# Optimization experiments

Measured on AMD Instinct MI355X. Metric: run time of the kernel, lower is better.

## Reference

```python
import jax, jax.numpy as jnp
import numpy as np

N_NODES = 50000
N_EDGES = 1600000
D = 128


def setup_inputs() -> dict:
    key = jax.random.key(0)
    ks = jax.random.split(key, 12)
    feats = jax.random.normal(ks[0], (N_NODES, D), dtype=jnp.float32)
    src = jax.random.randint(ks[1], (N_EDGES,), 0, N_NODES)
    dst = jax.random.randint(ks[2], (N_EDGES,), 0, N_NODES)
    s = 1.0 / np.sqrt(D)
    inp = {"feats": feats, "src": src, "dst": dst}
    for i, k0 in enumerate(range(3, 12, 3)):
        inp[f"w_self{i}"] = jax.random.normal(ks[k0], (D, D), dtype=jnp.float32) * s
        inp[f"w_neigh{i}"] = jax.random.normal(ks[k0 + 1], (D, D), dtype=jnp.float32) * s
        inp[f"b{i}"] = jnp.zeros((D,), dtype=jnp.float32)
    return inp


def _sage_layer(h, src, dst, deg, w_self, w_neigh, b, act):
    # mean aggregation over incoming edges: gather src feats, scatter-sum to dst
    neigh_sum = jax.ops.segment_sum(h[src], dst, num_segments=N_NODES)  # [N, d]
    neigh = neigh_sum / deg[:, None]  # zero-degree nodes stay 0 (deg clamped to 1)
    out = h @ w_self + neigh @ w_neigh + b
    return jax.nn.relu(out) if act else out


def reference(feats, src, dst, w_self0, w_neigh0, b0, w_self1, w_neigh1, b1, w_self2, w_neigh2, b2):
    ones = jnp.ones((src.shape[0],), dtype=feats.dtype)
    deg = jax.ops.segment_sum(ones, dst, num_segments=N_NODES)
    deg = jnp.maximum(deg, 1.0)
    h = _sage_layer(feats, src, dst, deg, w_self0, w_neigh0, b0, True)
    h = _sage_layer(h, src, dst, deg, w_self1, w_neigh1, b1, True)
    h = _sage_layer(h, src, dst, deg, w_self2, w_neigh2, b2, False)
    return h
```

## Files before the change

kernel.cpp:

```cpp
#include <hip/hip_runtime.h>
#include <hip/hip_bf16.h>

#define N_NODES 50000
#define N_EDGES 1600000
#define DF 128
#define EPB 2500
#define B1 640
#define NBIN 196

typedef __attribute__((ext_vector_type(8))) short short8v;
typedef __attribute__((ext_vector_type(4))) float float4v;

__device__ __forceinline__ ushort bf16rne(float f) {
    uint u = __float_as_uint(f);
    return (ushort)((u + 0x7fffu + ((u >> 16) & 1u)) >> 16);
}


__global__ __launch_bounds__(256) void h1_kernel(const int* __restrict__ dst,
                                                 int* __restrict__ gh) {
    __shared__ int hist[NBIN];
    const int tid = threadIdx.x;
    const int blk = blockIdx.x;
    if (tid < NBIN) hist[tid] = 0;
    __syncthreads();
    const int lo = blk * EPB, hiE = min(lo + EPB, N_EDGES);
    for (int i = lo + tid; i < hiE; i += 256) atomicAdd(&hist[dst[i] >> 8], 1);
    __syncthreads();
    if (tid < NBIN) gh[tid * B1 + blk] = hist[tid];
}

__global__ __launch_bounds__(256) void scanA_kernel(int* __restrict__ gh,
                                                    int* __restrict__ rowtot) {
    __shared__ int buf[256];
    __shared__ int carry_s;
    const int tid = threadIdx.x;
    const int d = blockIdx.x;
    if (tid == 0) carry_s = 0;
    __syncthreads();
    for (int base = 0; base < B1; base += 256) {
        int idx = base + tid;
        int v = (idx < B1) ? gh[d * B1 + idx] : 0;
        buf[tid] = v;
        __syncthreads();
#pragma unroll
        for (int off = 1; off < 256; off <<= 1) {
            int t = (tid >= off) ? buf[tid - off] : 0;
            __syncthreads();
            buf[tid] += t;
            __syncthreads();
        }
        int carry = carry_s;
        if (idx < B1) gh[d * B1 + idx] = carry + buf[tid] - v;
        int tot = buf[255];
        __syncthreads();
        if (tid == 0) carry_s = carry + tot;
        __syncthreads();
    }
    if (tid == 0) rowtot[d] = carry_s;
}

__global__ __launch_bounds__(256) void scanB_kernel(const int* __restrict__ rowtot,
                                                    int* __restrict__ rowbase) {
    __shared__ int buf[256];
    const int tid = threadIdx.x;
    int v = (tid < NBIN) ? rowtot[tid] : 0;
    buf[tid] = v;
    __syncthreads();
#pragma unroll
    for (int off = 1; off < 256; off <<= 1) {
        int t = (tid >= off) ? buf[tid - off] : 0;
        __syncthreads();
        buf[tid] += t;
        __syncthreads();
    }
    if (tid < NBIN) rowbase[tid] = buf[tid] - v;
    if (tid == 0) rowbase[NBIN] = buf[255];
}

__global__ __launch_bounds__(256) void scatter1_kernel(const int* __restrict__ src,
                                                       const int* __restrict__ dst,
                                                       const int* __restrict__ gh,
                                                       const int* __restrict__ rowbase,
                                                       uint2* __restrict__ tmp) {
    __shared__ int cur[NBIN];
    const int tid = threadIdx.x;
    const int blk = blockIdx.x;
    if (tid < NBIN) cur[tid] = rowbase[tid] + gh[tid * B1 + blk];
    __syncthreads();
    const int lo = blk * EPB, hiE = min(lo + EPB, N_EDGES);
    for (int i = lo + tid; i < hiE; i += 256) {
        int d = dst[i];
        int pos = atomicAdd(&cur[d >> 8], 1);
        uint2 v;
        v.x = (uint)src[i];
        v.y = (uint)d;
        tmp[pos] = v;
    }
}

__global__ __launch_bounds__(256) void pass2_kernel(const uint2* __restrict__ tmp,
                                                    const int* __restrict__ rowbase,
                                                    int* __restrict__ deg,
                                                    int* __restrict__ rstart,
                                                    int* __restrict__ adj,
                                                    int* __restrict__ counter) {
    __shared__ int hist[256];
    __shared__ int sbuf[256];
    __shared__ int cur2[256];
    __shared__ int base_s;
    const int tid = threadIdx.x;
    const int hi = blockIdx.x;
    const int s = rowbase[hi], e = rowbase[hi + 1];
    hist[tid] = 0;
    __syncthreads();
    for (int i = s + tid; i < e; i += 256) atomicAdd(&hist[tmp[i].y & 255u], 1);
    __syncthreads();
    int h = hist[tid];
    int v = (h + 3) & ~3;
    sbuf[tid] = v;
    __syncthreads();
#pragma unroll
    for (int off = 1; off < 256; off <<= 1) {
        int t = (tid >= off) ? sbuf[tid - off] : 0;
        __syncthreads();
        sbuf[tid] += t;
        __syncthreads();
    }
    if (tid == 255) base_s = atomicAdd(counter, sbuf[255]);
    __syncthreads();
    int rs = base_s + sbuf[tid] - v;
    int n = hi * 256 + tid;
    if (n < N_NODES) {
        deg[n] = h;
        rstart[n] = rs;
    }
    cur2[tid] = rs;
    __syncthreads();
    for (int i = s + tid; i < e; i += 256) {
        uint2 t2 = tmp[i];
        int pos = atomicAdd(&cur2[t2.y & 255u], 1);
        adj[pos] = (int)t2.x;
    }
}


__global__ __launch_bounds__(256) void conv_kernel(const float* __restrict__ h,
                                                   ushort* __restrict__ hb) {
    int i = blockIdx.x * 256 + threadIdx.x;
    const int total = N_NODES * DF / 4;
    if (i < total) {
        float4 v = ((const float4*)h)[i];
        ushort4 o;
        o.x = bf16rne(v.x); o.y = bf16rne(v.y);
        o.z = bf16rne(v.z); o.w = bf16rne(v.w);
        ((ushort4*)hb)[i] = o;
    }
}


__global__ __launch_bounds__(256) void wprep_kernel(const float* __restrict__ wS,
                                                    const float* __restrict__ wN,
                                                    ushort* __restrict__ Wt) {
    int idx = blockIdx.x * 256 + threadIdx.x;
    if (idx < 128 * 256) {
        int c = idx >> 8;
        int k = idx & 255;
        float v = (k < 128) ? wS[k * 128 + c] : wN[(k - 128) * 128 + c];
        Wt[c * 256 + k] = bf16rne(v);
    }
}


__global__ __launch_bounds__(256) void agg_kernel(const ushort* __restrict__ hb,
                                                  const int* __restrict__ rstart,
                                                  const int* __restrict__ degv,
                                                  const int* __restrict__ adj,
                                                  ushort* __restrict__ neighb) {
    const int wave = threadIdx.x >> 6;
    const int lane = threadIdx.x & 63;
    const int n = blockIdx.x * 4 + wave;
    if (n >= N_NODES) return;
    const int s = rstart[n];
    const int d = degv[n];
    const int off = lane * 2;
    float ax[8], ay[8];
#pragma unroll
    for (int j = 0; j < 8; j++) { ax[j] = 0.f; ay[j] = 0.f; }
    int i = 0;
    for (; i + 8 <= d; i += 8) {
        int4 a0 = *(const int4*)&adj[s + i];
        int4 a1 = *(const int4*)&adj[s + i + 4];
        uint u0 = *(const uint*)&hb[(size_t)a0.x * DF + off];
        uint u1 = *(const uint*)&hb[(size_t)a0.y * DF + off];
        uint u2 = *(const uint*)&hb[(size_t)a0.z * DF + off];
        uint u3 = *(const uint*)&hb[(size_t)a0.w * DF + off];
        uint u4 = *(const uint*)&hb[(size_t)a1.x * DF + off];
        uint u5 = *(const uint*)&hb[(size_t)a1.y * DF + off];
        uint u6 = *(const uint*)&hb[(size_t)a1.z * DF + off];
        uint u7 = *(const uint*)&hb[(size_t)a1.w * DF + off];
        ax[0] += __uint_as_float(u0 << 16); ay[0] += __uint_as_float(u0 & 0xffff0000u);
        ax[1] += __uint_as_float(u1 << 16); ay[1] += __uint_as_float(u1 & 0xffff0000u);
        ax[2] += __uint_as_float(u2 << 16); ay[2] += __uint_as_float(u2 & 0xffff0000u);
        ax[3] += __uint_as_float(u3 << 16); ay[3] += __uint_as_float(u3 & 0xffff0000u);
        ax[4] += __uint_as_float(u4 << 16); ay[4] += __uint_as_float(u4 & 0xffff0000u);
        ax[5] += __uint_as_float(u5 << 16); ay[5] += __uint_as_float(u5 & 0xffff0000u);
        ax[6] += __uint_as_float(u6 << 16); ay[6] += __uint_as_float(u6 & 0xffff0000u);
        ax[7] += __uint_as_float(u7 << 16); ay[7] += __uint_as_float(u7 & 0xffff0000u);
    }
    for (; i < d; i++) {
        int s0 = adj[s + i];
        uint u = *(const uint*)&hb[(size_t)s0 * DF + off];
        ax[0] += __uint_as_float(u << 16);
        ay[0] += __uint_as_float(u & 0xffff0000u);
    }
    float sx = (ax[0] + ax[1]) + (ax[2] + ax[3]) + ((ax[4] + ax[5]) + (ax[6] + ax[7]));
    float sy = (ay[0] + ay[1]) + (ay[2] + ay[3]) + ((ay[4] + ay[5]) + (ay[6] + ay[7]));
    float inv = 1.0f / (float)(d < 1 ? 1 : d);
    ushort2 o;
    o.x = bf16rne(sx * inv);
    o.y = bf16rne(sy * inv);
    *(ushort2*)&neighb[(size_t)n * DF + off] = o;
}


template <bool RELU, bool FP32OUT>
__global__ __launch_bounds__(256, 2) void gemm_mfma(const ushort* __restrict__ hbin,
                                                    const ushort* __restrict__ neighb,
                                                    const ushort* __restrict__ Wt,
                                                    const float* __restrict__ bias,
                                                    float* __restrict__ out32,
                                                    ushort* __restrict__ outbf) {
    __shared__ ushort As[128 * 40];
    __shared__ ushort Bs[128 * 40];
    const int tid = threadIdx.x;
    const int lane = tid & 63;
    const int w = tid >> 6;
    const int wrow = w >> 1, wcol = w & 1;
    const int nbase = blockIdx.x * 128;
    const int l15 = lane & 15, l4 = lane >> 4;

    float4v acc[4][4];
#pragma unroll
    for (int i = 0; i < 4; i++)
#pragma unroll
        for (int j = 0; j < 4; j++) acc[i][j] = (float4v)0.f;

    for (int ks = 0; ks < 8; ++ks) {
        const int k0 = ks * 32;
        const ushort* Xsrc = (ks < 4) ? hbin : neighb;
        const int kk = k0 & 127;
        if (ks) __syncthreads();
#pragma unroll
        for (int j = 0; j < 2; j++) {
            int ch = tid + j * 256;
            int r = ch >> 2, cp = ch & 3;
            int gn = nbase + r;
            if (gn > N_NODES - 1) gn = N_NODES - 1;
            *(uint4*)&As[r * 40 + cp * 8] =
                *(const uint4*)&Xsrc[(size_t)gn * 128 + kk + cp * 8];
        }
#pragma unroll
        for (int j = 0; j < 2; j++) {
            int ch = tid + j * 256;
            int r = ch >> 2, cp = ch & 3;
            *(uint4*)&Bs[r * 40 + cp * 8] =
                *(const uint4*)&Wt[(size_t)r * 256 + k0 + cp * 8];
        }
        __syncthreads();
        short8v a[4], b[4];
#pragma unroll
        for (int i = 0; i < 4; i++)
            a[i] = *(const short8v*)&As[(wrow * 64 + i * 16 + l15) * 40 + l4 * 8];
#pragma unroll
        for (int j = 0; j < 4; j++)
            b[j] = *(const short8v*)&Bs[(wcol * 64 + j * 16 + l15) * 40 + l4 * 8];
#pragma unroll
        for (int i = 0; i < 4; i++)
#pragma unroll
            for (int j = 0; j < 4; j++)
                acc[i][j] = __builtin_amdgcn_mfma_f32_16x16x32_bf16(
                    a[i], b[j], acc[i][j], 0, 0, 0);
    }

#pragma unroll
    for (int j = 0; j < 4; j++) {
        int col = wcol * 64 + j * 16 + l15;
        float bv = bias[col];
#pragma unroll
        for (int i = 0; i < 4; i++) {
            int row0 = nbase + wrow * 64 + i * 16 + l4 * 4;
#pragma unroll
            for (int r = 0; r < 4; r++) {
                int row = row0 + r;
                if (row < N_NODES) {
                    float v = acc[i][j][r] + bv;
                    if (RELU) v = fmaxf(v, 0.f);
                    if (FP32OUT) {
                        out32[(size_t)row * 128 + col] = v;
                    } else {
                        outbf[(size_t)row * 128 + col] = bf16rne(v);
                    }
                }
            }
        }
    }
}


extern "C" void kernel_launch(void* const* d_in, const int* in_sizes, int n_in,
                              void* d_out, int out_size, void* d_ws, size_t ws_size,
                              hipStream_t stream) {
    const float* feats = (const float*)d_in[0];
    const int* src = (const int*)d_in[1];
    const int* dst = (const int*)d_in[2];
    const float* wS[3] = {(const float*)d_in[3], (const float*)d_in[6], (const float*)d_in[9]};
    const float* wN[3] = {(const float*)d_in[4], (const float*)d_in[7], (const float*)d_in[10]};
    const float* bb[3] = {(const float*)d_in[5], (const float*)d_in[8], (const float*)d_in[11]};
    float* out = (float*)d_out;

    char* p = (char*)d_ws;
    auto alloc = [&](size_t bytes) {
        char* r = p;
        p += (bytes + 255) & ~(size_t)255;
        return r;
    };
    ushort* hbA = (ushort*)alloc((size_t)N_NODES * DF * sizeof(ushort));
    ushort* hbB = (ushort*)alloc((size_t)N_NODES * DF * sizeof(ushort));
    ushort* neighb = (ushort*)alloc((size_t)N_NODES * DF * sizeof(ushort));
    ushort* Wt = (ushort*)alloc((size_t)3 * 128 * 256 * sizeof(ushort));
    uint2* tmp = (uint2*)alloc((size_t)N_EDGES * sizeof(uint2));
    int* gh = (int*)alloc((size_t)NBIN * B1 * sizeof(int));
    int* rowtot = (int*)alloc((size_t)NBIN * sizeof(int));
    int* rowbase = (int*)alloc((size_t)(NBIN + 1) * sizeof(int));
    int* deg = (int*)alloc((size_t)N_NODES * sizeof(int));
    int* rstart = (int*)alloc((size_t)N_NODES * sizeof(int));
    int* counter = (int*)alloc(sizeof(int));
    int* adj = (int*)alloc((size_t)(N_EDGES + 4 * N_NODES) * sizeof(int));

    const int CB = (N_NODES * DF / 4 + 255) / 256;
    const int WB = (128 * 256 + 255) / 256;

    hipMemsetAsync(counter, 0, sizeof(int), stream);
    h1_kernel<<<B1, 256, 0, stream>>>(dst, gh);
    scanA_kernel<<<NBIN, 256, 0, stream>>>(gh, rowtot);
    scanB_kernel<<<1, 256, 0, stream>>>(rowtot, rowbase);
    scatter1_kernel<<<B1, 256, 0, stream>>>(src, dst, gh, rowbase, tmp);
    pass2_kernel<<<NBIN, 256, 0, stream>>>(tmp, rowbase, deg, rstart, adj, counter);

    wprep_kernel<<<WB, 256, 0, stream>>>(wS[0], wN[0], Wt);
    wprep_kernel<<<WB, 256, 0, stream>>>(wS[1], wN[1], Wt + 128 * 256);
    wprep_kernel<<<WB, 256, 0, stream>>>(wS[2], wN[2], Wt + 2 * 128 * 256);
    conv_kernel<<<CB, 256, 0, stream>>>(feats, hbA);

    const int AGG_GRID = (N_NODES + 3) / 4;
    const int GB = (N_NODES + 127) / 128;

    agg_kernel<<<AGG_GRID, 256, 0, stream>>>(hbA, rstart, deg, adj, neighb);
    gemm_mfma<true, false><<<GB, 256, 0, stream>>>(hbA, neighb, Wt, bb[0], nullptr, hbB);
    agg_kernel<<<AGG_GRID, 256, 0, stream>>>(hbB, rstart, deg, adj, neighb);
    gemm_mfma<true, false><<<GB, 256, 0, stream>>>(hbB, neighb, Wt + 128 * 256, bb[1], nullptr, hbA);
    agg_kernel<<<AGG_GRID, 256, 0, stream>>>(hbA, rstart, deg, adj, neighb);
    gemm_mfma<false, true><<<GB, 256, 0, stream>>>(hbA, neighb, Wt + 2 * 128 * 256, bb[2], out, nullptr);
}
```

Before: 371.3 us.

## Gather four neighbors per wave with 16-byte loads; shrink GEMM row tile

The aggregation kernel now splits each wave into four quarter-waves. Each quarter handles a different neighbor and loads 16-byte feature chunks instead of 4-byte ones, and the partial sums are combined with cross-lane shuffles before a single vectorized store. This is meant to raise memory-level parallelism and cut the number of load instructions per gathered row. Separately, the GEMM tile shrinks from 128 to 64 rows per block, doubling the grid so more blocks cover the GPU, at the cost of reloading weights more often and doing fewer MFMAs per block.

```diff
diff --git a/kernel.cpp b/kernel.cpp
--- a/kernel.cpp
+++ b/kernel.cpp
@@ -183,44 +183,59 @@
     if (n >= N_NODES) return;
     const int s = rstart[n];
     const int d = degv[n];
-    const int off = lane * 2;
-    float ax[8], ay[8];
-#pragma unroll
-    for (int j = 0; j < 8; j++) { ax[j] = 0.f; ay[j] = 0.f; }
+    const int q = lane >> 4;
+    const int f = lane & 15;
+    const size_t foff = (size_t)(f * 8);
+
+    float acc[8];
+#pragma unroll
+    for (int j = 0; j < 8; j++) acc[j] = 0.f;
+
+#define GATHER_ADD(EIDX)                                                    \
+    {                                                                       \
+        int e_ = adj[(EIDX)];                                               \
+        uint4 u_ = *(const uint4*)&hb[(size_t)e_ * DF + foff];              \
+        acc[0] += __uint_as_float(u_.x << 16);                              \
+        acc[1] += __uint_as_float(u_.x & 0xffff0000u);                      \
+        acc[2] += __uint_as_float(u_.y << 16);                              \
+        acc[3] += __uint_as_float(u_.y & 0xffff0000u);                      \
+        acc[4] += __uint_as_float(u_.z << 16);                              \
+        acc[5] += __uint_as_float(u_.z & 0xffff0000u);                      \
+        acc[6] += __uint_as_float(u_.w << 16);                              \
+        acc[7] += __uint_as_float(u_.w & 0xffff0000u);                      \
+    }
+
     int i = 0;
-    for (; i + 8 <= d; i += 8) {
-        int4 a0 = *(const int4*)&adj[s + i];
-        int4 a1 = *(const int4*)&adj[s + i + 4];
-        uint u0 = *(const uint*)&hb[(size_t)a0.x * DF + off];
-        uint u1 = *(const uint*)&hb[(size_t)a0.y * DF + off];
-        uint u2 = *(const uint*)&hb[(size_t)a0.z * DF + off];
-        uint u3 = *(const uint*)&hb[(size_t)a0.w * DF + off];
-        uint u4 = *(const uint*)&hb[(size_t)a1.x * DF + off];
-        uint u5 = *(const uint*)&hb[(size_t)a1.y * DF + off];
-        uint u6 = *(const uint*)&hb[(size_t)a1.z * DF + off];
-        uint u7 = *(const uint*)&hb[(size_t)a1.w * DF + off];
-        ax[0] += __uint_as_float(u0 << 16); ay[0] += __uint_as_float(u0 & 0xffff0000u);
-        ax[1] += __uint_as_float(u1 << 16); ay[1] += __uint_as_float(u1 & 0xffff0000u);
-        ax[2] += __uint_as_float(u2 << 16); ay[2] += __uint_as_float(u2 & 0xffff0000u);
-        ax[3] += __uint_as_float(u3 << 16); ay[3] += __uint_as_float(u3 & 0xffff0000u);
-        ax[4] += __uint_as_float(u4 << 16); ay[4] += __uint_as_float(u4 & 0xffff0000u);
-        ax[5] += __uint_as_float(u5 << 16); ay[5] += __uint_as_float(u5 & 0xffff0000u);
-        ax[6] += __uint_as_float(u6 << 16); ay[6] += __uint_as_float(u6 & 0xffff0000u);
-        ax[7] += __uint_as_float(u7 << 16); ay[7] += __uint_as_float(u7 & 0xffff0000u);
-    }
-    for (; i < d; i++) {
-        int s0 = adj[s + i];
-        uint u = *(const uint*)&hb[(size_t)s0 * DF + off];
-        ax[0] += __uint_as_float(u << 16);
-        ay[0] += __uint_as_float(u & 0xffff0000u);
-    }
-    float sx = (ax[0] + ax[1]) + (ax[2] + ax[3]) + ((ax[4] + ax[5]) + (ax[6] + ax[7]));
-    float sy = (ay[0] + ay[1]) + (ay[2] + ay[3]) + ((ay[4] + ay[5]) + (ay[6] + ay[7]));
-    float inv = 1.0f / (float)(d < 1 ? 1 : d);
-    ushort2 o;
-    o.x = bf16rne(sx * inv);
-    o.y = bf16rne(sy * inv);
-    *(ushort2*)&neighb[(size_t)n * DF + off] = o;
+    for (; i + 16 <= d; i += 16) {
+        GATHER_ADD(s + i + q)
+        GATHER_ADD(s + i + 4 + q)
+        GATHER_ADD(s + i + 8 + q)
+        GATHER_ADD(s + i + 12 + q)
+    }
+    for (; i + 4 <= d; i += 4) {
+        GATHER_ADD(s + i + q)
+    }
+    if (i < d) {
+        int r = d - i;
+        if (q < r) GATHER_ADD(s + i + q)
+    }
+#undef GATHER_ADD
+
+#pragma unroll
+    for (int j = 0; j < 8; j++) {
+        acc[j] += __shfl_xor(acc[j], 16, 64);
+        acc[j] += __shfl_xor(acc[j], 32, 64);
+    }
+
+    if (q == 0) {
+        float inv = 1.0f / (float)(d < 1 ? 1 : d);
+        uint4 o;
+        o.x = (uint)bf16rne(acc[0] * inv) | ((uint)bf16rne(acc[1] * inv) << 16);
+        o.y = (uint)bf16rne(acc[2] * inv) | ((uint)bf16rne(acc[3] * inv) << 16);
+        o.z = (uint)bf16rne(acc[4] * inv) | ((uint)bf16rne(acc[5] * inv) << 16);
+        o.w = (uint)bf16rne(acc[6] * inv) | ((uint)bf16rne(acc[7] * inv) << 16);
+        *(uint4*)&neighb[(size_t)n * DF + foff] = o;
+    }
 }
 
 
@@ -231,30 +246,27 @@
                                                     const float* __restrict__ bias,
                                                     float* __restrict__ out32,
                                                     ushort* __restrict__ outbf) {
-    __shared__ ushort As[128 * 40];
+    __shared__ ushort As[64 * 40];
     __shared__ ushort Bs[128 * 40];
     const int tid = threadIdx.x;
     const int lane = tid & 63;
     const int w = tid >> 6;
-    const int wrow = w >> 1, wcol = w & 1;
-    const int nbase = blockIdx.x * 128;
+    const int nbase = blockIdx.x * 64;
     const int l15 = lane & 15, l4 = lane >> 4;
 
-    float4v acc[4][4];
+    float4v acc[4][2];
 #pragma unroll
     for (int i = 0; i < 4; i++)
 #pragma unroll
-        for (int j = 0; j < 4; j++) acc[i][j] = (float4v)0.f;
+        for (int j = 0; j < 2; j++) acc[i][j] = (float4v)0.f;
 
     for (int ks = 0; ks < 8; ++ks) {
         const int k0 = ks * 32;
         const ushort* Xsrc = (ks < 4) ? hbin : neighb;
         const int kk = k0 & 127;
         if (ks) __syncthreads();
-#pragma unroll
-        for (int j = 0; j < 2; j++) {
-            int ch = tid + j * 256;
-            int r = ch >> 2, cp = ch & 3;
+        {
+            int r = tid >> 2, cp = tid & 3;
             int gn = nbase + r;
             if (gn > N_NODES - 1) gn = N_NODES - 1;
             *(uint4*)&As[r * 40 + cp * 8] =
@@ -268,28 +280,28 @@
                 *(const uint4*)&Wt[(size_t)r * 256 + k0 + cp * 8];
         }
         __syncthreads();
-        short8v a[4], b[4];
+        short8v a[4], b[2];
 #pragma unroll
         for (int i = 0; i < 4; i++)
-            a[i] = *(const short8v*)&As[(wrow * 64 + i * 16 + l15) * 40 + l4 * 8];
-#pragma unroll
-        for (int j = 0; j < 4; j++)
-            b[j] = *(const short8v*)&Bs[(wcol * 64 + j * 16 + l15) * 40 + l4 * 8];
+            a[i] = *(const short8v*)&As[(i * 16 + l15) * 40 + l4 * 8];
+#pragma unroll
+        for (int j = 0; j < 2; j++)
+            b[j] = *(const short8v*)&Bs[(w * 32 + j * 16 + l15) * 40 + l4 * 8];
 #pragma unroll
         for (int i = 0; i < 4; i++)
 #pragma unroll
-            for (int j = 0; j < 4; j++)
+            for (int j = 0; j < 2; j++)
                 acc[i][j] = __builtin_amdgcn_mfma_f32_16x16x32_bf16(
                     a[i], b[j], acc[i][j], 0, 0, 0);
     }
 
 #pragma unroll
-    for (int j = 0; j < 4; j++) {
-        int col = wcol * 64 + j * 16 + l15;
+    for (int j = 0; j < 2; j++) {
+        int col = w * 32 + j * 16 + l15;
         float bv = bias[col];
 #pragma unroll
         for (int i = 0; i < 4; i++) {
-            int row0 = nbase + wrow * 64 + i * 16 + l4 * 4;
+            int row0 = nbase + i * 16 + l4 * 4;
 #pragma unroll
             for (int r = 0; r < 4; r++) {
                 int row = row0 + r;
@@ -354,7 +366,7 @@
     conv_kernel<<<CB, 256, 0, stream>>>(feats, hbA);
 
     const int AGG_GRID = (N_NODES + 3) / 4;
-    const int GB = (N_NODES + 127) / 128;
+    const int GB = (N_NODES + 63) / 64;
 
     agg_kernel<<<AGG_GRID, 256, 0, stream>>>(hbA, rstart, deg, adj, neighb);
     gemm_mfma<true, false><<<GB, 256, 0, stream>>>(hbA, neighb, Wt, bb[0], nullptr, hbB);
```

After: 345.6 us. 1.07x faster.
